# Performance work log

Measured on AMD Instinct MI355X. Metric: run time of the kernel, lower is better.

## Reference

```python
import jax, jax.numpy as jnp
import numpy as np

IN_FEATURES = 4096
OUT_FEATURES = 8192
LUT_SIZE = 65536  # 256 * 256 two-level codebook


def setup_inputs() -> dict:
    key = jax.random.key(0)
    k_x, k_b, k_f, k_s, k_l = jax.random.split(key, 5)
    x = jax.random.normal(k_x, (2, 256, IN_FEATURES), dtype=jnp.float32)
    base_idx = jax.random.randint(k_b, (OUT_FEATURES, IN_FEATURES), 0, 256, dtype=jnp.int32)
    fine_idx = jax.random.randint(k_f, (OUT_FEATURES, IN_FEATURES), 0, 256, dtype=jnp.int32)
    scale = jax.random.uniform(k_s, (OUT_FEATURES, 1), dtype=jnp.float32)
    lut = jax.random.normal(k_l, (LUT_SIZE,), dtype=jnp.float32)
    return {"x": x, "base_idx": base_idx, "fine_idx": fine_idx, "scale": scale, "lut": lut}


def reference(x, base_idx, fine_idx, scale, lut):
    # Two-level LUT dequant: combined 16-bit index = base*256 + fine
    combined_idx = base_idx * 256 + fine_idx              # [out, in] int32
    weights = lut[combined_idx] * scale                   # [out, in] fp32, per-row scale
    # F.linear(x, weights) == x @ weights.T
    return jnp.einsum('bsi,oi->bso', x, weights)
```

## Files before the change

### kernel.cpp

```cpp
#include <hip/hip_runtime.h>

typedef unsigned short ushort_t;
typedef unsigned int   uint32;
typedef __attribute__((ext_vector_type(8)))  short short8;
typedef __attribute__((ext_vector_type(4)))  float floatx4;
typedef __attribute__((ext_vector_type(16))) float floatx16;

#define IN_F   4096
#define OUT_F  8192
#define M_TOT  512

__device__ __forceinline__ ushort_t f2bf(float f) {
    uint32 u = __builtin_bit_cast(uint32, f);
    u += 0x7FFFu + ((u >> 16) & 1u);
    return (ushort_t)(u >> 16);
}
__device__ __forceinline__ uint32 pack2bf(float a, float b) {
    return (uint32)f2bf(a) | ((uint32)f2bf(b) << 16);
}

__global__ void cvt_x_kernel(const float* __restrict__ x, ushort_t* __restrict__ xb) {
    int i = (blockIdx.x * 256 + threadIdx.x) * 8;
    float4 v0 = *(const float4*)(x + i);
    float4 v1 = *(const float4*)(x + i + 4);
    short8 s;
    s[0] = (short)f2bf(v0.x); s[1] = (short)f2bf(v0.y);
    s[2] = (short)f2bf(v0.z); s[3] = (short)f2bf(v0.w);
    s[4] = (short)f2bf(v1.x); s[5] = (short)f2bf(v1.y);
    s[6] = (short)f2bf(v1.z); s[7] = (short)f2bf(v1.w);
    *(short8*)(xb + i) = s;
}

__global__ __launch_bounds__(1024, 4)
void dequant_kernel(const int* __restrict__ base_idx, const int* __restrict__ fine_idx,
                    const float* __restrict__ lut, ushort_t* __restrict__ wq)
{
    __shared__ ushort_t sh_lut[65536];
    const int tid = threadIdx.x;
    for (int i = tid * 4; i < 65536; i += 1024 * 4) {
        float4 v = *(const float4*)(lut + i);
        *(uint32*)&sh_lut[i]     = pack2bf(v.x, v.y);
        *(uint32*)&sh_lut[i + 2] = pack2bf(v.z, v.w);
    }

    const int row   = blockIdx.x * 32 + (tid >> 5);
    const int kbase = blockIdx.y * 2048 + (tid & 31) * 4;
    const int* bp = base_idx + (size_t)row * IN_F + kbase;
    const int* fp = fine_idx + (size_t)row * IN_F + kbase;
    ushort_t*  op = wq       + (size_t)row * IN_F + kbase;

    int4 cb[2][4], cf[2][4];
#pragma unroll
    for (int u = 0; u < 4; ++u) {
        cb[0][u] = *(const int4*)(bp + u * 128);
        cf[0][u] = *(const int4*)(fp + u * 128);
    }
#pragma unroll
    for (int u = 0; u < 4; ++u) {
        cb[1][u] = *(const int4*)(bp + (4 + u) * 128);
        cf[1][u] = *(const int4*)(fp + (4 + u) * 128);
    }
    __syncthreads();

#pragma unroll
    for (int b = 0; b < 4; ++b) {
        const int cur = b & 1;
#pragma unroll
        for (int u = 0; u < 4; ++u) {
            uint32 w0 = (uint32)sh_lut[(cb[cur][u].x << 8) + cf[cur][u].x]
                      | ((uint32)sh_lut[(cb[cur][u].y << 8) + cf[cur][u].y] << 16);
            uint32 w1 = (uint32)sh_lut[(cb[cur][u].z << 8) + cf[cur][u].z]
                      | ((uint32)sh_lut[(cb[cur][u].w << 8) + cf[cur][u].w] << 16);
            uint2 wv; wv.x = w0; wv.y = w1;
            *(uint2*)(op + (size_t)(b * 4 + u) * 128) = wv;
        }
        if (b + 2 < 4) {
#pragma unroll
            for (int u = 0; u < 4; ++u) {
                cb[cur][u] = *(const int4*)(bp + ((b + 2) * 4 + u) * 128);
                cf[cur][u] = *(const int4*)(fp + ((b + 2) * 4 + u) * 128);
            }
        }
    }
}

#define BK 128
__global__ __launch_bounds__(256, 2)
void gemm_split_kernel(const ushort_t* __restrict__ xb, const ushort_t* __restrict__ wq,
                       float* __restrict__ part)
{
    __shared__ ushort_t shA[128 * BK];
    __shared__ ushort_t shB[128 * BK];

    const int tid  = threadIdx.x;
    const int wave = tid >> 6;
    const int m0   = blockIdx.x * 128;
    const int n0   = blockIdx.y * 128;
    const int kz   = blockIdx.z * (IN_F / 2);

    const int g = (tid & 15) ^ ((tid >> 4) & 7);
    const ushort_t* aBase = xb + (size_t)(m0 + (tid >> 4)) * IN_F + kz + g * 8;
    const ushort_t* bBase = wq + (size_t)(n0 + (tid >> 4)) * IN_F + kz + g * 8;
    typedef __attribute__((address_space(3))) ushort_t lds_us;
    typedef const __attribute__((address_space(1))) void gvoid;
    lds_us* sA3 = (lds_us*)shA;
    lds_us* sB3 = (lds_us*)shB;

    const int lane = tid & 63;
    const int l31  = lane & 31;
    const int lhi  = lane >> 5;
    const int qm   = wave & 1;
    const int qn   = wave >> 1;
    const int rx   = l31 & 7;

    floatx16 acc[2][2];
    const floatx16 z16 = {0.f,0.f,0.f,0.f,0.f,0.f,0.f,0.f,0.f,0.f,0.f,0.f,0.f,0.f,0.f,0.f};
    acc[0][0] = z16; acc[0][1] = z16; acc[1][0] = z16; acc[1][1] = z16;

    for (int kb = 0; kb < IN_F / 2; kb += BK) {
#pragma unroll
        for (int i = 0; i < 8; ++i) {
            __builtin_amdgcn_global_load_lds((gvoid*)(aBase + (size_t)i * 16 * IN_F + kb),
                (__attribute__((address_space(3))) void*)(sA3 + i * 2048 + wave * 512),
                16, 0, 0);
            __builtin_amdgcn_global_load_lds((gvoid*)(bBase + (size_t)i * 16 * IN_F + kb),
                (__attribute__((address_space(3))) void*)(sB3 + i * 2048 + wave * 512),
                16, 0, 0);
        }
        __syncthreads();

#pragma unroll
        for (int ks = 0; ks < 8; ++ks) {
            const int p = ((2 * ks + lhi) ^ rx) * 8;
            short8 a0 = *(const short8*)&shA[(qm * 64 +      l31) * BK + p];
            short8 a1 = *(const short8*)&shA[(qm * 64 + 32 + l31) * BK + p];
            short8 b0 = *(const short8*)&shB[(qn * 64 +      l31) * BK + p];
            short8 b1 = *(const short8*)&shB[(qn * 64 + 32 + l31) * BK + p];
            acc[0][0] = __builtin_amdgcn_mfma_f32_32x32x16_bf16(a0, b0, acc[0][0], 0, 0, 0);
            acc[0][1] = __builtin_amdgcn_mfma_f32_32x32x16_bf16(a0, b1, acc[0][1], 0, 0, 0);
            acc[1][0] = __builtin_amdgcn_mfma_f32_32x32x16_bf16(a1, b0, acc[1][0], 0, 0, 0);
            acc[1][1] = __builtin_amdgcn_mfma_f32_32x32x16_bf16(a1, b1, acc[1][1], 0, 0, 0);
        }
        __syncthreads();
    }

    float* pz = part + (size_t)blockIdx.z * M_TOT * OUT_F;
#pragma unroll
    for (int nt = 0; nt < 2; ++nt) {
        const int col = n0 + qn * 64 + nt * 32 + l31;
#pragma unroll
        for (int mt = 0; mt < 2; ++mt) {
            const int rbase = m0 + qm * 64 + mt * 32 + 4 * lhi;
#pragma unroll
            for (int reg = 0; reg < 16; ++reg) {
                const int row = rbase + (reg & 3) + 8 * (reg >> 2);
                pz[(size_t)row * OUT_F + col] = acc[mt][nt][reg];
            }
        }
    }
}

__global__ void reduce_kernel(const float* __restrict__ p0, const float* __restrict__ p1,
                              const float* __restrict__ scale, float* __restrict__ out)
{
    const int i = (blockIdx.x * 256 + threadIdx.x) * 4;
    float4 a = *(const float4*)(p0 + i);
    float4 b = *(const float4*)(p1 + i);
    float4 s = *(const float4*)(scale + (i & (OUT_F - 1)));
    float4 r;
    r.x = (a.x + b.x) * s.x;
    r.y = (a.y + b.y) * s.y;
    r.z = (a.z + b.z) * s.z;
    r.w = (a.w + b.w) * s.w;
    *(float4*)(out + i) = r;
}

__global__ __launch_bounds__(256)
void gemm_full_kernel(const ushort_t* __restrict__ xb, const ushort_t* __restrict__ wq,
                      const float* __restrict__ scale, float* __restrict__ out)
{
    __shared__ ushort_t shA[128 * BK];
    __shared__ ushort_t shB[128 * BK];

    const int tid  = threadIdx.x;
    const int wave = tid >> 6;
    const int m0   = blockIdx.x * 128;
    const int n0   = blockIdx.y * 128;

    const int g = (tid & 15) ^ ((tid >> 4) & 7);
    const ushort_t* aBase = xb + (size_t)(m0 + (tid >> 4)) * IN_F + g * 8;
    const ushort_t* bBase = wq + (size_t)(n0 + (tid >> 4)) * IN_F + g * 8;
    typedef __attribute__((address_space(3))) ushort_t lds_us;
    typedef const __attribute__((address_space(1))) void gvoid;
    lds_us* sA3 = (lds_us*)shA;
    lds_us* sB3 = (lds_us*)shB;

    const int lane = tid & 63;
    const int l31  = lane & 31;
    const int lhi  = lane >> 5;
    const int qm   = wave & 1;
    const int qn   = wave >> 1;
    const int rx   = l31 & 7;

    floatx16 acc[2][2];
    const floatx16 z16 = {0.f,0.f,0.f,0.f,0.f,0.f,0.f,0.f,0.f,0.f,0.f,0.f,0.f,0.f,0.f,0.f};
    acc[0][0] = z16; acc[0][1] = z16; acc[1][0] = z16; acc[1][1] = z16;

    for (int kb = 0; kb < IN_F; kb += BK) {
#pragma unroll
        for (int i = 0; i < 8; ++i) {
            __builtin_amdgcn_global_load_lds((gvoid*)(aBase + (size_t)i * 16 * IN_F + kb),
                (__attribute__((address_space(3))) void*)(sA3 + i * 2048 + wave * 512), 16, 0, 0);
            __builtin_amdgcn_global_load_lds((gvoid*)(bBase + (size_t)i * 16 * IN_F + kb),
                (__attribute__((address_space(3))) void*)(sB3 + i * 2048 + wave * 512), 16, 0, 0);
        }
        __syncthreads();
#pragma unroll
        for (int ks = 0; ks < 8; ++ks) {
            const int p = ((2 * ks + lhi) ^ rx) * 8;
            short8 a0 = *(const short8*)&shA[(qm * 64 +      l31) * BK + p];
            short8 a1 = *(const short8*)&shA[(qm * 64 + 32 + l31) * BK + p];
            short8 b0 = *(const short8*)&shB[(qn * 64 +      l31) * BK + p];
            short8 b1 = *(const short8*)&shB[(qn * 64 + 32 + l31) * BK + p];
            acc[0][0] = __builtin_amdgcn_mfma_f32_32x32x16_bf16(a0, b0, acc[0][0], 0, 0, 0);
            acc[0][1] = __builtin_amdgcn_mfma_f32_32x32x16_bf16(a0, b1, acc[0][1], 0, 0, 0);
            acc[1][0] = __builtin_amdgcn_mfma_f32_32x32x16_bf16(a1, b0, acc[1][0], 0, 0, 0);
            acc[1][1] = __builtin_amdgcn_mfma_f32_32x32x16_bf16(a1, b1, acc[1][1], 0, 0, 0);
        }
        __syncthreads();
    }
#pragma unroll
    for (int nt = 0; nt < 2; ++nt) {
        const int col = n0 + qn * 64 + nt * 32 + l31;
        const float sc = scale[col];
#pragma unroll
        for (int mt = 0; mt < 2; ++mt) {
            const int rbase = m0 + qm * 64 + mt * 32 + 4 * lhi;
#pragma unroll
            for (int reg = 0; reg < 16; ++reg) {
                const int row = rbase + (reg & 3) + 8 * (reg >> 2);
                out[(size_t)row * OUT_F + col] = acc[mt][nt][reg] * sc;
            }
        }
    }
}

#define NB  32
#define FBK 128
#define WS  136
#define NITER (IN_F / FBK)
template<bool XBF16>
__global__ __launch_bounds__(1024, 4)
void ghost_kernel(const float* __restrict__ xf, const ushort_t* __restrict__ xb,
                  const int* __restrict__ base_idx, const int* __restrict__ fine_idx,
                  const float* __restrict__ scale, const float* __restrict__ lut,
                  float* __restrict__ out)
{
    __shared__ ushort_t sh_lut[65536];
    __shared__ ushort_t sh_w[2][NB * WS];
    const int tid = threadIdx.x;
    const int n0  = blockIdx.x * NB;
    for (int i = tid * 4; i < 65536; i += 1024 * 4) {
        float4 v = *(const float4*)(lut + i);
        sh_lut[i + 0] = f2bf(v.x); sh_lut[i + 1] = f2bf(v.y);
        sh_lut[i + 2] = f2bf(v.z); sh_lut[i + 3] = f2bf(v.w);
    }
    const int sn  = tid >> 5;
    const int skq = (tid & 31) * 4;
    const int* bp = base_idx + (size_t)(n0 + sn) * IN_F + skq;
    const int* fp = fine_idx + (size_t)(n0 + sn) * IN_F + skq;
    __syncthreads();
    int4 pb = *(const int4*)(bp);
    int4 pf = *(const int4*)(fp);
    {
        uint32 w0 = (uint32)sh_lut[(pb.x << 8) + pf.x] | ((uint32)sh_lut[(pb.y << 8) + pf.y] << 16);
        uint32 w1 = (uint32)sh_lut[(pb.z << 8) + pf.z] | ((uint32)sh_lut[(pb.w << 8) + pf.w] << 16);
        uint2 wv; wv.x = w0; wv.y = w1;
        *(uint2*)&sh_w[0][sn * WS + skq] = wv;
    }
    pb = *(const int4*)(bp + FBK);
    pf = *(const int4*)(fp + FBK);
    __syncthreads();
    const int lane = tid & 63;
    const int wave = tid >> 6;
    const int l16  = lane & 15;
    const int quad = lane >> 4;
    floatx4 acc[2][2];
    const floatx4 zero = {0.f, 0.f, 0.f, 0.f};
    acc[0][0] = zero; acc[0][1] = zero; acc[1][0] = zero; acc[1][1] = zero;
    const int mrow = wave * 32 + l16;
    const ushort_t* xrow  = XBF16 ? (xb + (size_t)mrow * IN_F + quad * 8) : (const ushort_t*)nullptr;
    const float*    xrowf = XBF16 ? (const float*)nullptr : (xf + (size_t)mrow * IN_F + quad * 8);
    for (int t = 0; t < NITER; ++t) {
        const int k0 = t * FBK;
        {
            uint32 w0 = (uint32)sh_lut[(pb.x << 8) + pf.x] | ((uint32)sh_lut[(pb.y << 8) + pf.y] << 16);
            uint32 w1 = (uint32)sh_lut[(pb.z << 8) + pf.z] | ((uint32)sh_lut[(pb.w << 8) + pf.w] << 16);
            uint2 wv; wv.x = w0; wv.y = w1;
            *(uint2*)&sh_w[(t + 1) & 1][sn * WS + skq] = wv;
        }
        {
            const int kk = (t + 2 < NITER ? t + 2 : NITER - 1) * FBK;
            pb = *(const int4*)(bp + kk);
            pf = *(const int4*)(fp + kk);
        }
        const ushort_t* wb = sh_w[t & 1];
#pragma unroll
        for (int ks = 0; ks < 4; ++ks) {
            const int kk = k0 + ks * 32;
            short8 b0 = *(const short8*)&wb[l16        * WS + ks * 32 + quad * 8];
            short8 b1 = *(const short8*)&wb[(16 + l16) * WS + ks * 32 + quad * 8];
            short8 a0, a1;
            if (XBF16) {
                a0 = *(const short8*)(xrow + kk);
                a1 = *(const short8*)(xrow + (size_t)16 * IN_F + kk);
            } else {
                const float* p0 = xrowf + kk;
                const float* p1 = xrowf + (size_t)16 * IN_F + kk;
                float4 u0 = *(const float4*)p0, u1 = *(const float4*)(p0 + 4);
                float4 v0 = *(const float4*)p1, v1 = *(const float4*)(p1 + 4);
                a0[0] = (short)f2bf(u0.x); a0[1] = (short)f2bf(u0.y);
                a0[2] = (short)f2bf(u0.z); a0[3] = (short)f2bf(u0.w);
                a0[4] = (short)f2bf(u1.x); a0[5] = (short)f2bf(u1.y);
                a0[6] = (short)f2bf(u1.z); a0[7] = (short)f2bf(u1.w);
                a1[0] = (short)f2bf(v0.x); a1[1] = (short)f2bf(v0.y);
                a1[2] = (short)f2bf(v0.z); a1[3] = (short)f2bf(v0.w);
                a1[4] = (short)f2bf(v1.x); a1[5] = (short)f2bf(v1.y);
                a1[6] = (short)f2bf(v1.z); a1[7] = (short)f2bf(v1.w);
            }
            acc[0][0] = __builtin_amdgcn_mfma_f32_16x16x32_bf16(a0, b0, acc[0][0], 0, 0, 0);
            acc[0][1] = __builtin_amdgcn_mfma_f32_16x16x32_bf16(a0, b1, acc[0][1], 0, 0, 0);
            acc[1][0] = __builtin_amdgcn_mfma_f32_16x16x32_bf16(a1, b0, acc[1][0], 0, 0, 0);
            acc[1][1] = __builtin_amdgcn_mfma_f32_16x16x32_bf16(a1, b1, acc[1][1], 0, 0, 0);
        }
        __syncthreads();
    }
#pragma unroll
    for (int nf = 0; nf < 2; ++nf) {
        const int col = n0 + nf * 16 + l16;
        const float sc = scale[col];
#pragma unroll
        for (int f = 0; f < 2; ++f) {
            const int r0 = wave * 32 + f * 16 + quad * 4;
#pragma unroll
            for (int r = 0; r < 4; ++r) {
                out[(size_t)(r0 + r) * OUT_F + col] = acc[f][nf][r] * sc;
            }
        }
    }
}

extern "C" void kernel_launch(void* const* d_in, const int* in_sizes, int n_in,
                              void* d_out, int out_size, void* d_ws, size_t ws_size,
                              hipStream_t stream) {
    const float* x      = (const float*)d_in[0];
    const int*   bidx   = (const int*)d_in[1];
    const int*   fidx   = (const int*)d_in[2];
    const float* scale  = (const float*)d_in[3];
    const float* lut    = (const float*)d_in[4];
    float*       out    = (float*)d_out;

    const size_t xb_bytes = (size_t)M_TOT * IN_F * sizeof(ushort_t);
    const size_t wq_bytes = (size_t)OUT_F * IN_F * sizeof(ushort_t);
    const size_t pt_bytes = (size_t)M_TOT * OUT_F * sizeof(float);

    if (ws_size >= xb_bytes + wq_bytes + 2 * pt_bytes) {
        ushort_t* xbuf = (ushort_t*)d_ws;
        ushort_t* wbuf = (ushort_t*)((char*)d_ws + xb_bytes);
        float*    part = (float*)((char*)d_ws + xb_bytes + wq_bytes);
        cvt_x_kernel<<<1024, 256, 0, stream>>>(x, xbuf);
        dequant_kernel<<<dim3(256, 2), 1024, 0, stream>>>(bidx, fidx, lut, wbuf);
        gemm_split_kernel<<<dim3(4, 64, 2), 256, 0, stream>>>(xbuf, wbuf, part);
        reduce_kernel<<<(M_TOT * OUT_F) / (256 * 4), 256, 0, stream>>>(
            part, part + (size_t)M_TOT * OUT_F, scale, out);
    } else if (ws_size >= xb_bytes + wq_bytes) {
        ushort_t* xbuf = (ushort_t*)d_ws;
        ushort_t* wbuf = (ushort_t*)((char*)d_ws + xb_bytes);
        cvt_x_kernel<<<1024, 256, 0, stream>>>(x, xbuf);
        dequant_kernel<<<dim3(256, 2), 1024, 0, stream>>>(bidx, fidx, lut, wbuf);
        gemm_full_kernel<<<dim3(4, 64), 256, 0, stream>>>(xbuf, wbuf, scale, out);
    } else if (ws_size >= xb_bytes) {
        ushort_t* xbuf = (ushort_t*)d_ws;
        cvt_x_kernel<<<1024, 256, 0, stream>>>(x, xbuf);
        ghost_kernel<true><<<OUT_F / NB, 1024, 0, stream>>>(x, xbuf, bidx, fidx, scale, lut, out);
    } else {
        ghost_kernel<false><<<OUT_F / NB, 1024, 0, stream>>>(x, nullptr, bidx, fidx, scale, lut, out);
    }
}
```

Before: 364.4 us.

## Halve dequant grid so each block covers full rows with 4-deep prefetch ring

The dequant kernel now launches 256 blocks instead of 512, with each block handling full 4096-wide rows. This halves the number of times the 64K-entry LUT is loaded and converted into shared memory. Each thread now processes 8 contiguous indices per step and writes 16-byte stores, with a 4-slot rotating register prefetch for the index loads. The cost is fewer blocks and therefore less parallelism, plus more registers held per thread for the prefetch ring.

```diff
diff --git a/kernel.cpp b/kernel.cpp
--- a/kernel.cpp
+++ b/kernel.cpp
@@ -37,50 +37,50 @@
 {
     __shared__ ushort_t sh_lut[65536];
     const int tid = threadIdx.x;
+#pragma unroll
     for (int i = tid * 4; i < 65536; i += 1024 * 4) {
         float4 v = *(const float4*)(lut + i);
         *(uint32*)&sh_lut[i]     = pack2bf(v.x, v.y);
         *(uint32*)&sh_lut[i + 2] = pack2bf(v.z, v.w);
     }
 
-    const int row   = blockIdx.x * 32 + (tid >> 5);
-    const int kbase = blockIdx.y * 2048 + (tid & 31) * 4;
-    const int* bp = base_idx + (size_t)row * IN_F + kbase;
-    const int* fp = fine_idx + (size_t)row * IN_F + kbase;
-    ushort_t*  op = wq       + (size_t)row * IN_F + kbase;
-
-    int4 cb[2][4], cf[2][4];
-#pragma unroll
-    for (int u = 0; u < 4; ++u) {
-        cb[0][u] = *(const int4*)(bp + u * 128);
-        cf[0][u] = *(const int4*)(fp + u * 128);
-    }
-#pragma unroll
-    for (int u = 0; u < 4; ++u) {
-        cb[1][u] = *(const int4*)(bp + (4 + u) * 128);
-        cf[1][u] = *(const int4*)(fp + (4 + u) * 128);
+    const int row = blockIdx.x * 32 + (tid >> 5);
+    const int c0  = (tid & 31) * 8;
+    const int* bp = base_idx + (size_t)row * IN_F + c0;
+    const int* fp = fine_idx + (size_t)row * IN_F + c0;
+    ushort_t*  op = wq       + (size_t)row * IN_F + c0;
+
+    int4 cb[4][2], cf[4][2];
+#pragma unroll
+    for (int d = 0; d < 4; ++d) {
+        cb[d][0] = *(const int4*)(bp + d * 256);
+        cb[d][1] = *(const int4*)(bp + d * 256 + 4);
+        cf[d][0] = *(const int4*)(fp + d * 256);
+        cf[d][1] = *(const int4*)(fp + d * 256 + 4);
     }
     __syncthreads();
 
 #pragma unroll
-    for (int b = 0; b < 4; ++b) {
-        const int cur = b & 1;
-#pragma unroll
-        for (int u = 0; u < 4; ++u) {
-            uint32 w0 = (uint32)sh_lut[(cb[cur][u].x << 8) + cf[cur][u].x]
-                      | ((uint32)sh_lut[(cb[cur][u].y << 8) + cf[cur][u].y] << 16);
-            uint32 w1 = (uint32)sh_lut[(cb[cur][u].z << 8) + cf[cur][u].z]
-                      | ((uint32)sh_lut[(cb[cur][u].w << 8) + cf[cur][u].w] << 16);
-            uint2 wv; wv.x = w0; wv.y = w1;
-            *(uint2*)(op + (size_t)(b * 4 + u) * 128) = wv;
-        }
-        if (b + 2 < 4) {
-#pragma unroll
-            for (int u = 0; u < 4; ++u) {
-                cb[cur][u] = *(const int4*)(bp + ((b + 2) * 4 + u) * 128);
-                cf[cur][u] = *(const int4*)(fp + ((b + 2) * 4 + u) * 128);
-            }
-        }
+    for (int u = 0; u < 16; ++u) {
+        const int s = u & 3;
+        const int4 b0 = cb[s][0], b1 = cb[s][1];
+        const int4 f0 = cf[s][0], f1 = cf[s][1];
+        if (u + 4 < 16) {
+            cb[s][0] = *(const int4*)(bp + (u + 4) * 256);
+            cb[s][1] = *(const int4*)(bp + (u + 4) * 256 + 4);
+            cf[s][0] = *(const int4*)(fp + (u + 4) * 256);
+            cf[s][1] = *(const int4*)(fp + (u + 4) * 256 + 4);
+        }
+        uint32 w0 = (uint32)sh_lut[(b0.x << 8) + f0.x]
+                  | ((uint32)sh_lut[(b0.y << 8) + f0.y] << 16);
+        uint32 w1 = (uint32)sh_lut[(b0.z << 8) + f0.z]
+                  | ((uint32)sh_lut[(b0.w << 8) + f0.w] << 16);
+        uint32 w2 = (uint32)sh_lut[(b1.x << 8) + f1.x]
+                  | ((uint32)sh_lut[(b1.y << 8) + f1.y] << 16);
+        uint32 w3 = (uint32)sh_lut[(b1.z << 8) + f1.z]
+                  | ((uint32)sh_lut[(b1.w << 8) + f1.w] << 16);
+        uint4 wv; wv.x = w0; wv.y = w1; wv.z = w2; wv.w = w3;
+        *(uint4*)(op + u * 256) = wv;
     }
 }
 
@@ -369,7 +369,7 @@
         ushort_t* wbuf = (ushort_t*)((char*)d_ws + xb_bytes);
         float*    part = (float*)((char*)d_ws + xb_bytes + wq_bytes);
         cvt_x_kernel<<<1024, 256, 0, stream>>>(x, xbuf);
-        dequant_kernel<<<dim3(256, 2), 1024, 0, stream>>>(bidx, fidx, lut, wbuf);
+        dequant_kernel<<<256, 1024, 0, stream>>>(bidx, fidx, lut, wbuf);
         gemm_split_kernel<<<dim3(4, 64, 2), 256, 0, stream>>>(xbuf, wbuf, part);
         reduce_kernel<<<(M_TOT * OUT_F) / (256 * 4), 256, 0, stream>>>(
             part, part + (size_t)M_TOT * OUT_F, scale, out);
@@ -377,7 +377,7 @@
         ushort_t* xbuf = (ushort_t*)d_ws;
         ushort_t* wbuf = (ushort_t*)((char*)d_ws + xb_bytes);
         cvt_x_kernel<<<1024, 256, 0, stream>>>(x, xbuf);
-        dequant_kernel<<<dim3(256, 2), 1024, 0, stream>>>(bidx, fidx, lut, wbuf);
+        dequant_kernel<<<256, 1024, 0, stream>>>(bidx, fidx, lut, wbuf);
         gemm_full_kernel<<<dim3(4, 64), 256, 0, stream>>>(xbuf, wbuf, scale, out);
     } else if (ws_size >= xb_bytes) {
         ushort_t* xbuf = (ushort_t*)d_ws;
```

Measured after the change: 364.3 us. About the same (-0.0%).
